# Kernel tuning notes

Measured on AMD Instinct MI355X. Metric: run time of the kernel, lower is better.

Reference implementation:

```python
import jax, jax.numpy as jnp
import numpy as np

N_NODES = 50000
N_EDGES = 800000
EMB_DIM = 128
HID = 256


def setup_inputs() -> dict:
    key = jax.random.key(0)
    ks = jax.random.split(key, 9)
    src = jax.random.randint(ks[0], (N_EDGES,), 0, N_NODES, dtype=jnp.int32)
    dst = jax.random.randint(ks[1], (N_EDGES,), 0, N_NODES, dtype=jnp.int32)
    emb = jax.random.normal(ks[2], (N_NODES, EMB_DIM), dtype=jnp.float32)
    s1 = 1.0 / np.sqrt(EMB_DIM)
    s2 = 1.0 / np.sqrt(HID)
    W1 = jax.random.uniform(ks[3], (EMB_DIM, HID), jnp.float32, -s1, s1)
    b1 = jax.random.uniform(ks[4], (HID,), jnp.float32, -s1, s1)
    W2 = jax.random.uniform(ks[5], (HID, HID), jnp.float32, -s2, s2)
    b2 = jax.random.uniform(ks[6], (HID,), jnp.float32, -s2, s2)
    W3 = jax.random.uniform(ks[7], (HID, EMB_DIM), jnp.float32, -s2, s2)
    b3 = jax.random.uniform(ks[8], (EMB_DIM,), jnp.float32, -s2, s2)
    return {"src": src, "dst": dst, "emb": emb,
            "W1": W1, "b1": b1, "W2": W2, "b2": b2, "W3": W3, "b3": b3}


def _gin_conv(x, src, dst, W, b):
    # DGL GINConv 'max': (1+eps)*h + max over in-neighbors; eps=0 default.
    agg = jax.ops.segment_max(x[src], dst, num_segments=N_NODES)  # [N, d]
    agg = jnp.where(agg == -jnp.inf, 0.0, agg)  # isolated nodes -> 0 (DGL fill)
    return (x + agg) @ W + b


def reference(src, dst, emb, W1, b1, W2, b2, W3, b3):
    x = _gin_conv(emb, src, dst, W1, b1)
    x = jax.nn.relu(x)
    x = _gin_conv(x, src, dst, W2, b2)
    x = jax.nn.relu(x)
    out = _gin_conv(x, src, dst, W3, b3)  # no relu on last layer
    return out
```

## Files before the change

kernel.cpp:

```cpp
#include <hip/hip_runtime.h>
#include <math.h>

#define EMB 128
#define HIDN 256

typedef _Float16 half8 __attribute__((ext_vector_type(8)));
typedef _Float16 half4 __attribute__((ext_vector_type(4)));
typedef float f32x4 __attribute__((ext_vector_type(4)));


__global__ void zero_i32(int* p, int n) {
    int i = blockIdx.x * blockDim.x + threadIdx.x;
    if (i < n) p[i] = 0;
}

__global__ void hist_kernel(const int* __restrict__ dst, int E, int* __restrict__ cnt) {
    int i = blockIdx.x * blockDim.x + threadIdx.x;
    if (i < E) atomicAdd(&cnt[dst[i]], 1);
}

__global__ void scan_partial(const int* __restrict__ cnt, int* __restrict__ partials, int Nn) {
    __shared__ int red[256];
    const int b = blockIdx.x, t = threadIdx.x;
    const int base = b * 1024 + t * 4;
    int s = 0;
#pragma unroll
    for (int i = 0; i < 4; ++i)
        if (base + i < Nn) s += cnt[base + i];
    red[t] = s;
    __syncthreads();
    for (int d = 128; d > 0; d >>= 1) {
        if (t < d) red[t] += red[t + d];
        __syncthreads();
    }
    if (t == 0) partials[b] = red[0];
}

__global__ void scan_top(int* __restrict__ partials, int nB) {
    __shared__ int s[256];
    const int t = threadIdx.x;
    int orig = (t < nB) ? partials[t] : 0;
    s[t] = orig;
    __syncthreads();
    for (int d = 1; d < 256; d <<= 1) {
        int v = (t >= d) ? s[t - d] : 0;
        __syncthreads();
        s[t] += v;
        __syncthreads();
    }
    if (t < nB) partials[t] = s[t] - orig;
}

__global__ void scan_apply(const int* __restrict__ cnt, const int* __restrict__ pbase,
                           int* __restrict__ off, int* __restrict__ cur, int Nn, int E) {
    __shared__ int tsum[256];
    const int b = blockIdx.x, t = threadIdx.x;
    const int base = b * 1024 + t * 4;
    int c[4];
#pragma unroll
    for (int i = 0; i < 4; ++i) c[i] = (base + i < Nn) ? cnt[base + i] : 0;
    int s = c[0] + c[1] + c[2] + c[3];
    tsum[t] = s;
    __syncthreads();
    for (int d = 1; d < 256; d <<= 1) {
        int v = (t >= d) ? tsum[t - d] : 0;
        __syncthreads();
        tsum[t] += v;
        __syncthreads();
    }
    int run = pbase[b] + ((t == 0) ? 0 : tsum[t - 1]);
#pragma unroll
    for (int i = 0; i < 4; ++i) {
        int idx = base + i;
        if (idx < Nn) {
            off[idx] = run;
            cur[idx] = run;
            run += c[i];
        }
    }
    if (b == 0 && t == 0) off[Nn] = E;
}

__global__ void scatter_kernel(const int* __restrict__ src, const int* __restrict__ dst,
                               int E, int* __restrict__ cur, int* __restrict__ sorted) {
    int i = blockIdx.x * blockDim.x + threadIdx.x;
    if (i < E) {
        int d = dst[i];
        int p = atomicAdd(&cur[d], 1);
        sorted[p] = src[i];
    }
}


__global__ void f32_to_f16(const float* __restrict__ in, _Float16* __restrict__ out, int n4) {
    int i = blockIdx.x * blockDim.x + threadIdx.x;
    if (i < n4) {
        float4 v = *reinterpret_cast<const float4*>(in + (size_t)i * 4);
        half4 h;
        h[0] = (_Float16)v.x; h[1] = (_Float16)v.y;
        h[2] = (_Float16)v.z; h[3] = (_Float16)v.w;
        *reinterpret_cast<half4*>(out + (size_t)i * 4) = h;
    }
}

__global__ void pack_w(const float* __restrict__ W, _Float16* __restrict__ Wg, int K, int N) {
    int p = blockIdx.x * blockDim.x + threadIdx.x;
    if (p < (K / 8) * N) {
        int j = p / N, n = p - j * N;
        half8 h;
#pragma unroll
        for (int i = 0; i < 8; ++i) h[i] = (_Float16)W[(size_t)(j * 8 + i) * N + n];
        *reinterpret_cast<half8*>(Wg + (size_t)p * 8) = h;
    }
}


template <int K, int N, int NI, int NG, int OUT_F32, int RELU>
__global__ __launch_bounds__(512) void gin_layer(
    const _Float16* __restrict__ x, const int* __restrict__ off,
    const int* __restrict__ sorted, const _Float16* __restrict__ Wg,
    const float* __restrict__ bias, void* __restrict__ C, int Nn)
{
    __shared__ _Float16 sA[64 * K];

    const int tid  = threadIdx.x;
    const int wave = tid >> 6;
    const int lane = tid & 63;
    const int node0 = blockIdx.x * 64;

    constexpr int LPR = 64 / NG;
    const int g   = lane / LPR;
    const int col = (lane % LPR) * 8;
    const _Float16* xcol = x + col;

    for (int nd = 0; nd < 8; ++nd) {
        const int row = wave * 8 + nd;
        const int node = node0 + row;
        if (node >= Nn) break;
        const int beg = off[node];
        const int end = off[node + 1];

        half8 acc;
#pragma unroll
        for (int i = 0; i < 8; ++i) acc[i] = (_Float16)(-INFINITY);

        for (int eb = beg; eb < end; eb += 64) {
            const int cnt = min(64, end - eb);
            int myIdx = sorted[eb + (lane < cnt ? lane : cnt - 1)];
            const int nj = (cnt + NG - 1) / NG;
#pragma unroll 4
            for (int j = 0; j < nj; ++j) {
                int s = __shfl(myIdx, j * NG + g);
                half8 v = *reinterpret_cast<const half8*>(xcol + (size_t)s * K);
                acc = __builtin_elementwise_max(acc, v);
            }
        }

        union U { half8 h; int i[4]; };
        if (NG == 4) {
            U a, b; a.h = acc;
#pragma unroll
            for (int k = 0; k < 4; ++k) b.i[k] = __shfl_xor(a.i[k], 16);
            acc = __builtin_elementwise_max(a.h, b.h);
        }
        {
            U a, b; a.h = acc;
#pragma unroll
            for (int k = 0; k < 4; ++k) b.i[k] = __shfl_xor(a.i[k], 32);
            acc = __builtin_elementwise_max(a.h, b.h);
        }

        if (g == 0) {
            const bool hasEdges = (end > beg);
            half8 xv = *reinterpret_cast<const half8*>(xcol + (size_t)node * K);
            half8 o;
#pragma unroll
            for (int i = 0; i < 8; ++i)
                o[i] = (_Float16)((float)xv[i] + (hasEdges ? (float)acc[i] : 0.0f));
            const int j = lane;
            const int p = (j << 6) + (row ^ (j & 7));
            *reinterpret_cast<half8*>(&sA[p << 3]) = o;
        }
    }
    __syncthreads();

    const int r  = lane & 15;
    const int gq = lane >> 4;
    const int nb = wave * (N / 8);

    f32x4 acc2[4][NI];
#pragma unroll
    for (int mi = 0; mi < 4; ++mi)
#pragma unroll
        for (int ni = 0; ni < NI; ++ni) acc2[mi][ni] = (f32x4){0.f, 0.f, 0.f, 0.f};

    for (int k0 = 0; k0 < K; k0 += 32) {
        const int jb = (k0 >> 3) + gq;
        half8 aF[4];
#pragma unroll
        for (int mi = 0; mi < 4; ++mi) {
            int row = mi * 16 + r;
            int p = (jb << 6) + (row ^ (jb & 7));
            aF[mi] = *reinterpret_cast<const half8*>(&sA[p << 3]);
        }
        half8 bF[NI];
#pragma unroll
        for (int ni = 0; ni < NI; ++ni)
            bF[ni] = *reinterpret_cast<const half8*>(Wg + ((size_t)jb * N + nb + ni * 16 + r) * 8);
#pragma unroll
        for (int mi = 0; mi < 4; ++mi)
#pragma unroll
            for (int ni = 0; ni < NI; ++ni)
                acc2[mi][ni] = __builtin_amdgcn_mfma_f32_16x16x32_f16(aF[mi], bF[ni], acc2[mi][ni], 0, 0, 0);
    }

#pragma unroll
    for (int ni = 0; ni < NI; ++ni) {
        int colC = nb + ni * 16 + r;
        float bv = bias[colC];
#pragma unroll
        for (int mi = 0; mi < 4; ++mi) {
#pragma unroll
            for (int q = 0; q < 4; ++q) {
                int row = node0 + mi * 16 + (gq << 2) + q;
                if (row < Nn) {
                    float v = acc2[mi][ni][q] + bv;
                    if (RELU) v = fmaxf(v, 0.f);
                    if (OUT_F32) ((float*)C)[(size_t)row * N + colC] = v;
                    else         ((_Float16*)C)[(size_t)row * N + colC] = (_Float16)v;
                }
            }
        }
    }
}


extern "C" void kernel_launch(void* const* d_in, const int* in_sizes, int n_in,
                              void* d_out, int out_size, void* d_ws, size_t ws_size,
                              hipStream_t stream) {
    const int*   src = (const int*)d_in[0];
    const int*   dst = (const int*)d_in[1];
    const float* emb = (const float*)d_in[2];
    const float* W1  = (const float*)d_in[3];
    const float* b1  = (const float*)d_in[4];
    const float* W2  = (const float*)d_in[5];
    const float* b2  = (const float*)d_in[6];
    const float* W3  = (const float*)d_in[7];
    const float* b3  = (const float*)d_in[8];
    float* out = (float*)d_out;

    const int E  = in_sizes[0];
    const int Nn = in_sizes[2] / EMB;

    char* ws = (char*)d_ws;
    auto align256 = [](size_t x) { return (x + 255) & ~(size_t)255; };
    size_t p = 0;
    int* off      = (int*)(ws + p); p = align256(p + (size_t)(Nn + 1) * 4);
    int* cur      = (int*)(ws + p); p = align256(p + (size_t)(Nn + 1) * 4);
    int* partials = (int*)(ws + p); p = align256(p + 256 * 4);
    int* sorted   = (int*)(ws + p); p = align256(p + (size_t)E * 4);
    _Float16* buf0 = (_Float16*)(ws + p); p = align256(p + (size_t)Nn * HIDN * 2);
    _Float16* buf1 = (_Float16*)(ws + p); p = align256(p + (size_t)Nn * HIDN * 2);
    _Float16* Wg1  = (_Float16*)(ws + p); p = align256(p + (size_t)EMB * HIDN * 2);
    _Float16* Wg2  = (_Float16*)(ws + p); p = align256(p + (size_t)HIDN * HIDN * 2);
    _Float16* Wg3  = (_Float16*)(ws + p); p = align256(p + (size_t)HIDN * EMB * 2);

    const int nScanBlocks = (Nn + 1023) / 1024;
    zero_i32<<<(Nn + 255) / 256, 256, 0, stream>>>(cur, Nn);
    hist_kernel<<<(E + 255) / 256, 256, 0, stream>>>(dst, E, cur);
    scan_partial<<<nScanBlocks, 256, 0, stream>>>(cur, partials, Nn);
    scan_top<<<1, 256, 0, stream>>>(partials, nScanBlocks);
    scan_apply<<<nScanBlocks, 256, 0, stream>>>(cur, partials, off, cur, Nn, E);
    scatter_kernel<<<(E + 255) / 256, 256, 0, stream>>>(src, dst, E, cur, sorted);

    pack_w<<<(EMB / 8 * HIDN + 255) / 256, 256, 0, stream>>>(W1, Wg1, EMB, HIDN);
    pack_w<<<(HIDN / 8 * HIDN + 255) / 256, 256, 0, stream>>>(W2, Wg2, HIDN, HIDN);
    pack_w<<<(HIDN / 8 * EMB + 255) / 256, 256, 0, stream>>>(W3, Wg3, HIDN, EMB);
    f32_to_f16<<<(Nn * EMB / 4 + 255) / 256, 256, 0, stream>>>(emb, buf0, Nn * EMB / 4);

    const int blocks = (Nn + 63) / 64;

    gin_layer<128, 256, 2, 4, 0, 1><<<blocks, 512, 0, stream>>>(buf0, off, sorted, Wg1, b1, buf1, Nn);
    gin_layer<256, 256, 2, 2, 0, 1><<<blocks, 512, 0, stream>>>(buf1, off, sorted, Wg2, b2, buf0, Nn);
    gin_layer<256, 128, 1, 2, 1, 0><<<blocks, 512, 0, stream>>>(buf0, off, sorted, Wg3, b3, out, Nn);
}
```

Before: 342.7 us.

## Split fused GIN layer into column-sliced segment-max and separate MFMA GEMM

Replaces the fused aggregate+GEMM kernel with two kernels per layer. A column-sliced segment-max kernel assigns 32-column slices to separate blocks so that concurrently running blocks gather the same narrow column band, which is meant to improve L2 locality of the random gathers. It writes the result in a pre-tiled layout for a standalone MFMA GEMM that reads A directly from global memory. Neighbor indices are also stored as 16-bit to halve index traffic, which silently assumes fewer than 65536 nodes. The cost is an extra round-trip of the aggregated activations through global memory and more kernel launches.

```diff
diff --git a/kernel.cpp b/kernel.cpp
--- a/kernel.cpp
+++ b/kernel.cpp
@@ -7,6 +7,7 @@
 typedef _Float16 half8 __attribute__((ext_vector_type(8)));
 typedef _Float16 half4 __attribute__((ext_vector_type(4)));
 typedef float f32x4 __attribute__((ext_vector_type(4)));
+typedef unsigned short u16;
 
 
 __global__ void zero_i32(int* p, int n) {
@@ -82,12 +83,12 @@
 }
 
 __global__ void scatter_kernel(const int* __restrict__ src, const int* __restrict__ dst,
-                               int E, int* __restrict__ cur, int* __restrict__ sorted) {
+                               int E, int* __restrict__ cur, u16* __restrict__ sorted) {
     int i = blockIdx.x * blockDim.x + threadIdx.x;
     if (i < E) {
         int d = dst[i];
         int p = atomicAdd(&cur[d], 1);
-        sorted[p] = src[i];
+        sorted[p] = (u16)src[i];
     }
 }
 
@@ -115,108 +116,104 @@
 }
 
 
-template <int K, int N, int NI, int NG, int OUT_F32, int RELU>
-__global__ __launch_bounds__(512) void gin_layer(
+template <int K>
+__global__ __launch_bounds__(256) void seg_sliced(
     const _Float16* __restrict__ x, const int* __restrict__ off,
-    const int* __restrict__ sorted, const _Float16* __restrict__ Wg,
+    const u16* __restrict__ sorted, _Float16* __restrict__ xg, int Nn)
+{
+    constexpr int SL = K / 32;
+    const int slice = blockIdx.x % SL;
+    const int node  = (blockIdx.x / SL) * 4 + (threadIdx.x >> 6);
+    const int lane  = threadIdx.x & 63;
+    if (node >= Nn) return;
+    const int c0  = slice * 32;
+    const int g   = lane >> 2;
+    const int sub = lane & 3;
+    const _Float16* xcol = x + c0 + sub * 8;
+
+    const int beg = off[node];
+    const int end = off[node + 1];
+
+    half8 acc;
+#pragma unroll
+    for (int i = 0; i < 8; ++i) acc[i] = (_Float16)(-INFINITY);
+
+    for (int eb = beg; eb < end; eb += 64) {
+        const int cnt = min(64, end - eb);
+        int myIdx = sorted[eb + (lane < cnt ? lane : cnt - 1)];
+        const int nj = (cnt + 15) >> 4;
+#pragma unroll 2
+        for (int j = 0; j < nj; ++j) {
+            int s = __shfl(myIdx, j * 16 + g);
+            half8 v = *reinterpret_cast<const half8*>(xcol + (size_t)s * K);
+            acc = __builtin_elementwise_max(acc, v);
+        }
+    }
+
+    union U { half8 h; int i[4]; };
+#pragma unroll
+    for (int m = 4; m <= 32; m <<= 1) {
+        U a, b; a.h = acc;
+#pragma unroll
+        for (int k = 0; k < 4; ++k) b.i[k] = __shfl_xor(a.i[k], m);
+        acc = __builtin_elementwise_max(a.h, b.h);
+    }
+
+    if (lane < 4) {
+        const bool hasEdges = (end > beg);
+        half8 xv = *reinterpret_cast<const half8*>(x + (size_t)node * K + c0 + lane * 8);
+        half8 o;
+#pragma unroll
+        for (int i = 0; i < 8; ++i)
+            o[i] = (_Float16)((float)xv[i] + (hasEdges ? (float)acc[i] : 0.0f));
+        const int j = (c0 >> 3) + lane;
+        size_t gidx = ((size_t)(node >> 6) * (K / 8) + j) * 64 + (node & 63);
+        *reinterpret_cast<half8*>(xg + gidx * 8) = o;
+    }
+}
+
+
+template <int K, int N, int RB, int CB, int OUT_F32, int RELU>
+__global__ __launch_bounds__(256) void gemm_g(
+    const _Float16* __restrict__ xg, const _Float16* __restrict__ Wg,
     const float* __restrict__ bias, void* __restrict__ C, int Nn)
 {
-    __shared__ _Float16 sA[64 * K];
-
-    const int tid  = threadIdx.x;
-    const int wave = tid >> 6;
-    const int lane = tid & 63;
-    const int node0 = blockIdx.x * 64;
-
-    constexpr int LPR = 64 / NG;
-    const int g   = lane / LPR;
-    const int col = (lane % LPR) * 8;
-    const _Float16* xcol = x + col;
-
-    for (int nd = 0; nd < 8; ++nd) {
-        const int row = wave * 8 + nd;
-        const int node = node0 + row;
-        if (node >= Nn) break;
-        const int beg = off[node];
-        const int end = off[node + 1];
-
-        half8 acc;
-#pragma unroll
-        for (int i = 0; i < 8; ++i) acc[i] = (_Float16)(-INFINITY);
-
-        for (int eb = beg; eb < end; eb += 64) {
-            const int cnt = min(64, end - eb);
-            int myIdx = sorted[eb + (lane < cnt ? lane : cnt - 1)];
-            const int nj = (cnt + NG - 1) / NG;
-#pragma unroll 4
-            for (int j = 0; j < nj; ++j) {
-                int s = __shfl(myIdx, j * NG + g);
-                half8 v = *reinterpret_cast<const half8*>(xcol + (size_t)s * K);
-                acc = __builtin_elementwise_max(acc, v);
-            }
-        }
-
-        union U { half8 h; int i[4]; };
-        if (NG == 4) {
-            U a, b; a.h = acc;
-#pragma unroll
-            for (int k = 0; k < 4; ++k) b.i[k] = __shfl_xor(a.i[k], 16);
-            acc = __builtin_elementwise_max(a.h, b.h);
-        }
-        {
-            U a, b; a.h = acc;
-#pragma unroll
-            for (int k = 0; k < 4; ++k) b.i[k] = __shfl_xor(a.i[k], 32);
-            acc = __builtin_elementwise_max(a.h, b.h);
-        }
-
-        if (g == 0) {
-            const bool hasEdges = (end > beg);
-            half8 xv = *reinterpret_cast<const half8*>(xcol + (size_t)node * K);
-            half8 o;
-#pragma unroll
-            for (int i = 0; i < 8; ++i)
-                o[i] = (_Float16)((float)xv[i] + (hasEdges ? (float)acc[i] : 0.0f));
-            const int j = lane;
-            const int p = (j << 6) + (row ^ (j & 7));
-            *reinterpret_cast<half8*>(&sA[p << 3]) = o;
-        }
-    }
-    __syncthreads();
-
+    const int wave = threadIdx.x >> 6;
+    const int lane = threadIdx.x & 63;
+    const int wr = wave / CB, wc = wave % CB;
+    const int rowTile = blockIdx.x * RB + wr;
+    const int node0 = rowTile * 64;
     const int r  = lane & 15;
     const int gq = lane >> 4;
-    const int nb = wave * (N / 8);
-
-    f32x4 acc2[4][NI];
+    const int cb = wc * 64;
+
+    f32x4 acc[4][4];
 #pragma unroll
     for (int mi = 0; mi < 4; ++mi)
 #pragma unroll
-        for (int ni = 0; ni < NI; ++ni) acc2[mi][ni] = (f32x4){0.f, 0.f, 0.f, 0.f};
+        for (int ni = 0; ni < 4; ++ni) acc[mi][ni] = (f32x4){0.f, 0.f, 0.f, 0.f};
+
+    const _Float16* Ab = xg + (size_t)rowTile * K * 64;
 
     for (int k0 = 0; k0 < K; k0 += 32) {
         const int jb = (k0 >> 3) + gq;
-        half8 aF[4];
-#pragma unroll
-        for (int mi = 0; mi < 4; ++mi) {
-            int row = mi * 16 + r;
-            int p = (jb << 6) + (row ^ (jb & 7));
-            aF[mi] = *reinterpret_cast<const half8*>(&sA[p << 3]);
-        }
-        half8 bF[NI];
-#pragma unroll
-        for (int ni = 0; ni < NI; ++ni)
-            bF[ni] = *reinterpret_cast<const half8*>(Wg + ((size_t)jb * N + nb + ni * 16 + r) * 8);
+        half8 aF[4], bF[4];
 #pragma unroll
         for (int mi = 0; mi < 4; ++mi)
-#pragma unroll
-            for (int ni = 0; ni < NI; ++ni)
-                acc2[mi][ni] = __builtin_amdgcn_mfma_f32_16x16x32_f16(aF[mi], bF[ni], acc2[mi][ni], 0, 0, 0);
-    }
-
-#pragma unroll
-    for (int ni = 0; ni < NI; ++ni) {
-        int colC = nb + ni * 16 + r;
+            aF[mi] = *reinterpret_cast<const half8*>(Ab + (size_t)((jb << 6) + mi * 16 + r) * 8);
+#pragma unroll
+        for (int ni = 0; ni < 4; ++ni)
+            bF[ni] = *reinterpret_cast<const half8*>(Wg + ((size_t)jb * N + cb + ni * 16 + r) * 8);
+#pragma unroll
+        for (int mi = 0; mi < 4; ++mi)
+#pragma unroll
+            for (int ni = 0; ni < 4; ++ni)
+                acc[mi][ni] = __builtin_amdgcn_mfma_f32_16x16x32_f16(aF[mi], bF[ni], acc[mi][ni], 0, 0, 0);
+    }
+
+#pragma unroll
+    for (int ni = 0; ni < 4; ++ni) {
+        int colC = cb + ni * 16 + r;
         float bv = bias[colC];
 #pragma unroll
         for (int mi = 0; mi < 4; ++mi) {
@@ -224,7 +221,7 @@
             for (int q = 0; q < 4; ++q) {
                 int row = node0 + mi * 16 + (gq << 2) + q;
                 if (row < Nn) {
-                    float v = acc2[mi][ni][q] + bv;
+                    float v = acc[mi][ni][q] + bv;
                     if (RELU) v = fmaxf(v, 0.f);
                     if (OUT_F32) ((float*)C)[(size_t)row * N + colC] = v;
                     else         ((_Float16*)C)[(size_t)row * N + colC] = (_Float16)v;
@@ -251,6 +248,7 @@
 
     const int E  = in_sizes[0];
     const int Nn = in_sizes[2] / EMB;
+    const int nTiles = (Nn + 63) / 64;
 
     char* ws = (char*)d_ws;
     auto align256 = [](size_t x) { return (x + 255) & ~(size_t)255; };
@@ -258,9 +256,10 @@
     int* off      = (int*)(ws + p); p = align256(p + (size_t)(Nn + 1) * 4);
     int* cur      = (int*)(ws + p); p = align256(p + (size_t)(Nn + 1) * 4);
     int* partials = (int*)(ws + p); p = align256(p + 256 * 4);
-    int* sorted   = (int*)(ws + p); p = align256(p + (size_t)E * 4);
+    u16* sorted   = (u16*)(ws + p); p = align256(p + (size_t)E * 2);
     _Float16* buf0 = (_Float16*)(ws + p); p = align256(p + (size_t)Nn * HIDN * 2);
     _Float16* buf1 = (_Float16*)(ws + p); p = align256(p + (size_t)Nn * HIDN * 2);
+    _Float16* xg   = (_Float16*)(ws + p); p = align256(p + (size_t)nTiles * 64 * HIDN * 2);
     _Float16* Wg1  = (_Float16*)(ws + p); p = align256(p + (size_t)EMB * HIDN * 2);
     _Float16* Wg2  = (_Float16*)(ws + p); p = align256(p + (size_t)HIDN * HIDN * 2);
     _Float16* Wg3  = (_Float16*)(ws + p); p = align256(p + (size_t)HIDN * EMB * 2);
@@ -278,9 +277,14 @@
     pack_w<<<(HIDN / 8 * EMB + 255) / 256, 256, 0, stream>>>(W3, Wg3, HIDN, EMB);
     f32_to_f16<<<(Nn * EMB / 4 + 255) / 256, 256, 0, stream>>>(emb, buf0, Nn * EMB / 4);
 
-    const int blocks = (Nn + 63) / 64;
-
-    gin_layer<128, 256, 2, 4, 0, 1><<<blocks, 512, 0, stream>>>(buf0, off, sorted, Wg1, b1, buf1, Nn);
-    gin_layer<256, 256, 2, 2, 0, 1><<<blocks, 512, 0, stream>>>(buf1, off, sorted, Wg2, b2, buf0, Nn);
-    gin_layer<256, 128, 1, 2, 1, 0><<<blocks, 512, 0, stream>>>(buf0, off, sorted, Wg3, b3, out, Nn);
-}
+    const int nodeGroups = (Nn + 3) / 4;
+
+    seg_sliced<128><<<4 * nodeGroups, 256, 0, stream>>>(buf0, off, sorted, xg, Nn);
+    gemm_g<128, 256, 1, 4, 0, 1><<<nTiles, 256, 0, stream>>>(xg, Wg1, b1, buf1, Nn);
+
+    seg_sliced<256><<<8 * nodeGroups, 256, 0, stream>>>(buf1, off, sorted, xg, Nn);
+    gemm_g<256, 256, 1, 4, 0, 1><<<nTiles, 256, 0, stream>>>(xg, Wg2, b2, buf0, Nn);
+
+    seg_sliced<256><<<8 * nodeGroups, 256, 0, stream>>>(buf0, off, sorted, xg, Nn);
+    gemm_g<256, 128, 2, 2, 1, 0><<<(nTiles + 1) / 2, 256, 0, stream>>>(xg, Wg3, b3, out, Nn);
+}
```

New measurement: 499.0 us. +45.6%, slower.
